# Optimization experiments

Measured on AMD Instinct MI355X. Metric: run time of the kernel, lower is better.

The kernel has to match this reference:

```python
import jax, jax.numpy as jnp
import numpy as np

K = 3  # kernel_size=(3,3), flat all-ones structuring element


def _erode(x):
    # flat erosion = sliding-window min, SAME padding with +inf (geodesic)
    return jax.lax.reduce_window(x, float('inf'), jax.lax.min,
                                 (1, 1, K, K), (1, 1, 1, 1), 'SAME')


def _dilate(x):
    # flat dilation = sliding-window max, SAME padding with -inf
    return jax.lax.reduce_window(x, -float('inf'), jax.lax.max,
                                 (1, 1, K, K), (1, 1, 1, 1), 'SAME')


def setup_inputs() -> dict:
    key = jax.random.key(0)
    x = jax.random.uniform(key, (16, 3, 1024, 1024), dtype=jnp.float32)
    return {"x": x}


def reference(x) -> jnp.ndarray:
    # morphological opening: dilation(erosion(x)) with flat 3x3 SE,
    # applied per-channel (kernel repeated over channels in the original)
    return _dilate(_erode(x))
```

## Files before the change

kernel.cpp:

```cpp
#include <hip/hip_runtime.h>


#define W 1024
#define H 1024
#define ROWS 16
#define NT 256

typedef float nvec4 __attribute__((ext_vector_type(4)));

struct Row { float4 A, B; };

__global__ __launch_bounds__(NT, 2)
void open3x3_v5(const float* __restrict__ in, float* __restrict__ out) {
    const int t  = threadIdx.x;
    const int c0 = 4 * t;
    const int y0 = blockIdx.x * ROWS;
    const size_t imgoff = (size_t)blockIdx.y * (size_t)(W * H);
    const float* img  = in  + imgoff;
    float*       outp = out + imgoff;

    const float PINF = __builtin_inff();
    const float NINF = -__builtin_inff();
    const bool has_l = (c0 > 0);
    const bool has_r = (c0 + 4 < W);
    const int  cla   = has_l ? c0 - 2 : 0;
    const int  crb   = has_r ? c0 + 2 : W - 4;

    auto load_row = [&](int r) -> Row {
        Row R;
        if (r >= 0 && r < H) {
            const float* p = img + r * W;
            R.A = *(const float4*)(p + cla);
            R.B = *(const float4*)(p + crb);
        } else {
            R.A = make_float4(PINF, PINF, PINF, PINF);
            R.B = R.A;
        }
        return R;
    };

    auto hmin6 = [&](const Row& R, float hm[6]) {
        const float x0 = has_l ? R.A.x : PINF;
        const float x1 = has_l ? R.A.y : PINF;
        const float x2 = has_l ? R.A.z : R.A.x;
        const float x3 = has_l ? R.A.w : R.A.y;
        const float x4 = has_r ? R.B.x : R.B.z;
        const float x5 = has_r ? R.B.y : R.B.w;
        const float x6 = has_r ? R.B.z : PINF;
        const float x7 = has_r ? R.B.w : PINF;
        hm[0] = fminf(fminf(x0, x1), x2);
        hm[1] = fminf(fminf(x1, x2), x3);
        hm[2] = fminf(fminf(x2, x3), x4);
        hm[3] = fminf(fminf(x3, x4), x5);
        hm[4] = fminf(fminf(x4, x5), x6);
        hm[5] = fminf(fminf(x5, x6), x7);
    };

    auto erow = [&](int r, const float a[6], const float b[6], const float c[6], float e[6]) {
        if (r >= 0 && r < H) {
            #pragma unroll
            for (int i = 0; i < 6; i++) e[i] = fminf(fminf(a[i], b[i]), c[i]);
            if (!has_l) e[0] = NINF;
            if (!has_r) e[5] = NINF;
        } else {
            #pragma unroll
            for (int i = 0; i < 6; i++) e[i] = NINF;
        }
    };

    auto hmax4 = [&](const float e[6], float hx[4]) {
        #pragma unroll
        for (int i = 0; i < 4; i++) hx[i] = fmaxf(fmaxf(e[i], e[i + 1]), e[i + 2]);
    };

    Row r0 = load_row(y0 - 2);
    Row r1 = load_row(y0 - 1);
    Row r2 = load_row(y0);
    Row r3 = load_row(y0 + 1);
    Row buf[3];
    buf[0] = load_row(y0 + 2);
    buf[1] = load_row(y0 + 3);
    buf[2] = load_row(y0 + 4);
    __builtin_amdgcn_sched_barrier(0);

    float hmA[6], hmB[6], hmC[6], hmD[6];
    hmin6(r0, hmA); hmin6(r1, hmB); hmin6(r2, hmC); hmin6(r3, hmD);
    float e[6], hx0[4], hx1[4], hx2[4];
    erow(y0 - 1, hmA, hmB, hmC, e); hmax4(e, hx0);
    erow(y0,     hmB, hmC, hmD, e); hmax4(e, hx1);
    float hmP[6], hmQ[6], hmR[6];
    #pragma unroll
    for (int i = 0; i < 6; i++) { hmP[i] = hmC[i]; hmQ[i] = hmD[i]; }

    #pragma unroll
    for (int k = 0; k < ROWS; k++) {
        const int y = y0 + k;
        Row cur = buf[k % 3];
        if (k < ROWS - 3) buf[k % 3] = load_row(y + 5);
        __builtin_amdgcn_sched_barrier(0);

        hmin6(cur, hmR);
        erow(y + 1, hmP, hmQ, hmR, e);
        hmax4(e, hx2);

        nvec4 o;
        o.x = fmaxf(fmaxf(hx0[0], hx1[0]), hx2[0]);
        o.y = fmaxf(fmaxf(hx0[1], hx1[1]), hx2[1]);
        o.z = fmaxf(fmaxf(hx0[2], hx1[2]), hx2[2]);
        o.w = fmaxf(fmaxf(hx0[3], hx1[3]), hx2[3]);
        __builtin_nontemporal_store(o, (nvec4*)(outp + (size_t)y * W + c0));

        #pragma unroll
        for (int i = 0; i < 4; i++) { hx0[i] = hx1[i]; hx1[i] = hx2[i]; }
        #pragma unroll
        for (int i = 0; i < 6; i++) { hmP[i] = hmQ[i]; hmQ[i] = hmR[i]; }
    }
}

extern "C" void kernel_launch(void* const* d_in, const int* in_sizes, int n_in,
                              void* d_out, int out_size, void* d_ws, size_t ws_size,
                              hipStream_t stream) {
    const float* x = (const float*)d_in[0];
    float* out = (float*)d_out;
    dim3 grid(H / ROWS, 48);
    dim3 block(NT);
    open3x3_v5<<<grid, block, 0, stream>>>(x, out);
}
```

Baseline: 343.0 us.

## Compute one output row per block with strided row assignment

The kernel now has each block produce a single output row. It loads five input rows directly, with clamped addresses and an infinity mask, instead of streaming 16 rows through a rolling register buffer. Block indices are interleaved so that adjacent blocks work on rows far apart in the image. This trades the vertical reuse of loaded rows for far more parallelism and fewer registers, and relies on L2 to absorb the roughly fivefold redundant row reads. The interleaving may also spread memory traffic across channels, but it weakens the locality that L2 reuse between neighbouring rows depends on.

```diff
diff --git a/kernel.cpp b/kernel.cpp
--- a/kernel.cpp
+++ b/kernel.cpp
@@ -3,18 +3,16 @@
 
 #define W 1024
 #define H 1024
-#define ROWS 16
 #define NT 256
 
 typedef float nvec4 __attribute__((ext_vector_type(4)));
 
-struct Row { float4 A, B; };
-
-__global__ __launch_bounds__(NT, 2)
-void open3x3_v5(const float* __restrict__ in, float* __restrict__ out) {
+__global__ __launch_bounds__(NT)
+void open3x3_v6(const float* __restrict__ in, float* __restrict__ out) {
     const int t  = threadIdx.x;
     const int c0 = 4 * t;
-    const int y0 = blockIdx.x * ROWS;
+    const int bx = blockIdx.x;
+    const int y  = (bx & 7) * (H / 8) + (bx >> 3);
     const size_t imgoff = (size_t)blockIdx.y * (size_t)(W * H);
     const float* img  = in  + imgoff;
     float*       outp = out + imgoff;
@@ -26,95 +24,66 @@
     const int  cla   = has_l ? c0 - 2 : 0;
     const int  crb   = has_r ? c0 + 2 : W - 4;
 
-    auto load_row = [&](int r) -> Row {
-        Row R;
-        if (r >= 0 && r < H) {
-            const float* p = img + r * W;
-            R.A = *(const float4*)(p + cla);
-            R.B = *(const float4*)(p + crb);
-        } else {
-            R.A = make_float4(PINF, PINF, PINF, PINF);
-            R.B = R.A;
+    float4 A[5], B[5];
+    #pragma unroll
+    for (int i = 0; i < 5; i++) {
+        int r  = y - 2 + i;
+        int rc = r < 0 ? 0 : (r > H - 1 ? H - 1 : r);
+        const float* p = img + rc * W;
+        A[i] = *(const float4*)(p + cla);
+        B[i] = *(const float4*)(p + crb);
+    }
+
+    float hm[5][6];
+    #pragma unroll
+    for (int i = 0; i < 5; i++) {
+        const int r = y - 2 + i;
+        const bool rok = (r >= 0) && (r <= H - 1);
+        const float x0 = has_l ? A[i].x : PINF;
+        const float x1 = has_l ? A[i].y : PINF;
+        const float x2 = has_l ? A[i].z : A[i].x;
+        const float x3 = has_l ? A[i].w : A[i].y;
+        const float x4 = has_r ? B[i].x : B[i].z;
+        const float x5 = has_r ? B[i].y : B[i].w;
+        const float x6 = has_r ? B[i].z : PINF;
+        const float x7 = has_r ? B[i].w : PINF;
+        float h0 = fminf(fminf(x0, x1), x2);
+        float h1 = fminf(fminf(x1, x2), x3);
+        float h2 = fminf(fminf(x2, x3), x4);
+        float h3 = fminf(fminf(x3, x4), x5);
+        float h4 = fminf(fminf(x4, x5), x6);
+        float h5 = fminf(fminf(x5, x6), x7);
+        hm[i][0] = rok ? h0 : PINF;
+        hm[i][1] = rok ? h1 : PINF;
+        hm[i][2] = rok ? h2 : PINF;
+        hm[i][3] = rok ? h3 : PINF;
+        hm[i][4] = rok ? h4 : PINF;
+        hm[i][5] = rok ? h5 : PINF;
+    }
+
+    float e[3][6];
+    #pragma unroll
+    for (int j = 0; j < 3; j++) {
+        const int ey = y - 1 + j;
+        const bool eok = (ey >= 0) && (ey <= H - 1);
+        #pragma unroll
+        for (int i = 0; i < 6; i++) {
+            float v = fminf(fminf(hm[j][i], hm[j + 1][i]), hm[j + 2][i]);
+            e[j][i] = eok ? v : NINF;
         }
-        return R;
-    };
+        if (!has_l) e[j][0] = NINF;
+        if (!has_r) e[j][5] = NINF;
+    }
 
-    auto hmin6 = [&](const Row& R, float hm[6]) {
-        const float x0 = has_l ? R.A.x : PINF;
-        const float x1 = has_l ? R.A.y : PINF;
-        const float x2 = has_l ? R.A.z : R.A.x;
-        const float x3 = has_l ? R.A.w : R.A.y;
-        const float x4 = has_r ? R.B.x : R.B.z;
-        const float x5 = has_r ? R.B.y : R.B.w;
-        const float x6 = has_r ? R.B.z : PINF;
-        const float x7 = has_r ? R.B.w : PINF;
-        hm[0] = fminf(fminf(x0, x1), x2);
-        hm[1] = fminf(fminf(x1, x2), x3);
-        hm[2] = fminf(fminf(x2, x3), x4);
-        hm[3] = fminf(fminf(x3, x4), x5);
-        hm[4] = fminf(fminf(x4, x5), x6);
-        hm[5] = fminf(fminf(x5, x6), x7);
-    };
-
-    auto erow = [&](int r, const float a[6], const float b[6], const float c[6], float e[6]) {
-        if (r >= 0 && r < H) {
-            #pragma unroll
-            for (int i = 0; i < 6; i++) e[i] = fminf(fminf(a[i], b[i]), c[i]);
-            if (!has_l) e[0] = NINF;
-            if (!has_r) e[5] = NINF;
-        } else {
-            #pragma unroll
-            for (int i = 0; i < 6; i++) e[i] = NINF;
-        }
-    };
-
-    auto hmax4 = [&](const float e[6], float hx[4]) {
-        #pragma unroll
-        for (int i = 0; i < 4; i++) hx[i] = fmaxf(fmaxf(e[i], e[i + 1]), e[i + 2]);
-    };
-
-    Row r0 = load_row(y0 - 2);
-    Row r1 = load_row(y0 - 1);
-    Row r2 = load_row(y0);
-    Row r3 = load_row(y0 + 1);
-    Row buf[3];
-    buf[0] = load_row(y0 + 2);
-    buf[1] = load_row(y0 + 3);
-    buf[2] = load_row(y0 + 4);
-    __builtin_amdgcn_sched_barrier(0);
-
-    float hmA[6], hmB[6], hmC[6], hmD[6];
-    hmin6(r0, hmA); hmin6(r1, hmB); hmin6(r2, hmC); hmin6(r3, hmD);
-    float e[6], hx0[4], hx1[4], hx2[4];
-    erow(y0 - 1, hmA, hmB, hmC, e); hmax4(e, hx0);
-    erow(y0,     hmB, hmC, hmD, e); hmax4(e, hx1);
-    float hmP[6], hmQ[6], hmR[6];
+    nvec4 o;
     #pragma unroll
-    for (int i = 0; i < 6; i++) { hmP[i] = hmC[i]; hmQ[i] = hmD[i]; }
-
-    #pragma unroll
-    for (int k = 0; k < ROWS; k++) {
-        const int y = y0 + k;
-        Row cur = buf[k % 3];
-        if (k < ROWS - 3) buf[k % 3] = load_row(y + 5);
-        __builtin_amdgcn_sched_barrier(0);
-
-        hmin6(cur, hmR);
-        erow(y + 1, hmP, hmQ, hmR, e);
-        hmax4(e, hx2);
-
-        nvec4 o;
-        o.x = fmaxf(fmaxf(hx0[0], hx1[0]), hx2[0]);
-        o.y = fmaxf(fmaxf(hx0[1], hx1[1]), hx2[1]);
-        o.z = fmaxf(fmaxf(hx0[2], hx1[2]), hx2[2]);
-        o.w = fmaxf(fmaxf(hx0[3], hx1[3]), hx2[3]);
-        __builtin_nontemporal_store(o, (nvec4*)(outp + (size_t)y * W + c0));
-
-        #pragma unroll
-        for (int i = 0; i < 4; i++) { hx0[i] = hx1[i]; hx1[i] = hx2[i]; }
-        #pragma unroll
-        for (int i = 0; i < 6; i++) { hmP[i] = hmQ[i]; hmQ[i] = hmR[i]; }
+    for (int i = 0; i < 4; i++) {
+        float h0 = fmaxf(fmaxf(e[0][i], e[0][i + 1]), e[0][i + 2]);
+        float h1 = fmaxf(fmaxf(e[1][i], e[1][i + 1]), e[1][i + 2]);
+        float h2 = fmaxf(fmaxf(e[2][i], e[2][i + 1]), e[2][i + 2]);
+        o[i] = fmaxf(fmaxf(h0, h1), h2);
     }
+    __builtin_nontemporal_store(o, (nvec4*)(outp + (size_t)y * W + c0));
 }
 
 extern "C" void kernel_launch(void* const* d_in, const int* in_sizes, int n_in,
@@ -122,7 +91,7 @@
                               hipStream_t stream) {
     const float* x = (const float*)d_in[0];
     float* out = (float*)d_out;
-    dim3 grid(H / ROWS, 48);
+    dim3 grid(H, 48);
     dim3 block(NT);
-    open3x3_v5<<<grid, block, 0, stream>>>(x, out);
+    open3x3_v6<<<grid, block, 0, stream>>>(x, out);
 }
```

New measurement: 390.5 us. 13.8% more time.
